# Kernel tuning notes

Hardware: AMD Instinct MI355X
Metric: run time of the kernel (lower is better)

Reference implementation:

```python
import jax, jax.numpy as jnp
import numpy as np

N, D, H, F, T = 2048, 256, 4, 64, 64
HF = H * F


def setup_inputs() -> dict:
    key = jax.random.key(0)
    ks = jax.random.split(key, 24)
    f32 = jnp.float32
    emb = jax.random.normal(ks[0], (N, D), f32)
    y_as_x = jax.random.normal(ks[1], (N, T), f32)
    adj = (jax.random.uniform(ks[2], (N, N)) < 0.02).astype(f32)
    u = lambda k, shape, s: jax.random.uniform(k, shape, f32, -s, s)
    stdv = 1.0 / np.sqrt(HF)
    inp = dict(emb=emb, y_as_x=y_as_x, adj=adj)
    for i, p in enumerate(['pos', 'neg']):
        o = 3 + i * 6
        inp[p + '_w'] = u(ks[o], (D, HF), stdv)
        inp[p + '_wu'] = u(ks[o + 1], (H, F), 1.0)
        inp[p + '_wv'] = u(ks[o + 2], (H, F), 1.0)
        inp[p + '_b'] = u(ks[o + 3], (1, HF), stdv)
        inp[p + '_pw'] = u(ks[o + 4], (D, HF), 0.02)
        inp[p + '_pb'] = jnp.zeros((HF,), f32)
    inp['self_w'] = u(ks[15], (D, D), 0.02)
    inp['self_b'] = jnp.zeros((D,), f32)
    inp['mlp_pos_w'] = u(ks[16], (HF, D), 0.02)
    inp['mlp_pos_b'] = jnp.zeros((D,), f32)
    inp['mlp_neg_w'] = u(ks[17], (HF, D), 0.02)
    inp['mlp_neg_b'] = jnp.zeros((D,), f32)
    inp['sem_w1'] = u(ks[18], (D, D), 0.02)
    inp['sem_b1'] = jnp.zeros((D,), f32)
    inp['sem_w2'] = u(ks[19], (D, 1), 0.02)
    return inp


def _gat(x, mask, w, wu, wv, b, pw, pb):
    # x: [N,D], mask: [N,N] bool; multi-head GAT with dense masked softmax
    s = (x @ w).reshape(N, H, F).transpose(1, 0, 2)          # [H,N,F]
    f1 = jnp.einsum('hnf,hf->hn', s, wu)                     # u-score per node
    f2 = jnp.einsum('hnf,hf->hn', s, wv)                     # v-score per node
    logits = f1[:, None, :] + f2[:, :, None]                 # [H,N,N], i<-j
    logits = jax.nn.leaky_relu(logits, 0.2)
    masked = jnp.where(mask[None], logits, -1e9)
    attn = jnp.where(mask[None], jax.nn.softmax(masked, axis=2), 0.0)
    out = jnp.einsum('hij,hjf->hif', attn, s)                # [H,N,F]
    out = out.transpose(1, 0, 2).reshape(N, HF) + b
    return out + x @ pw + pb


def reference(emb, y_as_x, adj, pos_w, pos_wu, pos_wv, pos_b, pos_pw, pos_pb,
              neg_w, neg_wu, neg_wv, neg_b, neg_pw, neg_pb,
              self_w, self_b, mlp_pos_w, mlp_pos_b, mlp_neg_w, mlp_neg_b,
              sem_w1, sem_b1, sem_w2):
    # batched pairwise correlation (replaces the per-node Python loop)
    yc = y_as_x - y_as_x.mean(axis=1, keepdims=True)         # centered
    dot = yc @ yc.T                                          # [N,N]
    std = jnp.sqrt((yc ** 2).sum(axis=1) / (T - 1))          # torch std: ddof=1
    corr = dot / (std[:, None] * std[None, :])
    edge = adj != 0
    pos_mask = edge & (corr >= 0.1)
    neg_mask = edge & (corr < 0.1)

    pos_sup = _gat(emb, pos_mask, pos_w, pos_wu, pos_wv, pos_b, pos_pw, pos_pb)
    neg_sup = _gat(emb, neg_mask, neg_w, neg_wu, neg_wv, neg_b, neg_pw, neg_pb)

    sup = emb @ self_w + self_b
    pos_sup = pos_sup @ mlp_pos_w + mlp_pos_b
    neg_sup = neg_sup @ mlp_neg_w + mlp_neg_b

    all_emb = jnp.stack((sup, pos_sup, neg_sup), axis=1)     # [N,3,D]
    # semantic attention over the 3 relation channels
    wlog = jnp.tanh(all_emb @ sem_w1 + sem_b1) @ sem_w2      # [N,3,1]
    beta = jax.nn.softmax(wlog, axis=1)
    x = (beta * all_emb).sum(axis=1)                         # [N,D]
    # PairNorm PN-SI
    x = x - x.mean(axis=0)
    rownorm = jnp.sqrt(1e-6 + (x ** 2).sum(axis=1, keepdims=True))
    return x / rownorm
```

## Files before the change

kernel.cpp:

```cpp
#include <hip/hip_runtime.h>
#include <hip/hip_bf16.h>

#define KN  2048
#define KD  256
#define KH  4
#define KF  64
#define KT  64

typedef __attribute__((ext_vector_type(8))) short short8;
typedef __attribute__((ext_vector_type(4))) float floatx4;

__device__ __forceinline__ float wave_sum(float v) {
    #pragma unroll
    for (int o = 32; o > 0; o >>= 1) v += __shfl_xor(v, o, 64);
    return v;
}
__device__ __forceinline__ float wave_max(float v) {
    #pragma unroll
    for (int o = 32; o > 0; o >>= 1) v = fmaxf(v, __shfl_xor(v, o, 64));
    return v;
}
__device__ __forceinline__ short f2bs(float x) {
    union { __hip_bfloat16 h; short s; } u;
    u.h = __float2bfloat16(x);
    return u.s;
}

__global__ __launch_bounds__(256) void setup_kernel(const float* __restrict__ y,
                                                    float* __restrict__ ycs,
                                                    float* __restrict__ colsum) {
    int blk = blockIdx.x;
    if (blk < 512) {
        int w = threadIdx.x >> 6, lane = threadIdx.x & 63;
        int n = blk * 4 + w;
        float v = y[n * KT + lane];
        float mean = wave_sum(v) * (1.0f / KT);
        float yc = v - mean;
        float ss = wave_sum(yc * yc);
        ycs[n * KT + lane] = yc * rsqrtf(ss * (1.0f / (KT - 1)));
    } else {
        for (int j = threadIdx.x; j < 8 * KD; j += 256) colsum[j] = 0.0f;
    }
}

__device__ __forceinline__ void corr_body(const float* __restrict__ ycs,
                                          const float* __restrict__ adj,
                                          unsigned char* __restrict__ code,
                                          int blk, char* smem) {
    float (*As)[68] = (float(*)[68])smem;
    float (*Bs)[68] = (float(*)[68])(smem + 4352);
    int t = threadIdx.x;
    int tx = t & 15, ty = t >> 4;
    int j0 = (blk & 31) * 64, i0 = (blk >> 5) * 64;
    int ar = t >> 2, ac = (t & 3) * 4;
    float acc[4][4] = {};
    for (int kt = 0; kt < KT; kt += 16) {
        float4 a4 = *reinterpret_cast<const float4*>(&ycs[(size_t)(i0 + ar) * KT + kt + ac]);
        float4 b4 = *reinterpret_cast<const float4*>(&ycs[(size_t)(j0 + ar) * KT + kt + ac]);
        As[ac + 0][ar] = a4.x; As[ac + 1][ar] = a4.y; As[ac + 2][ar] = a4.z; As[ac + 3][ar] = a4.w;
        Bs[ac + 0][ar] = b4.x; Bs[ac + 1][ar] = b4.y; Bs[ac + 2][ar] = b4.z; Bs[ac + 3][ar] = b4.w;
        __syncthreads();
        #pragma unroll
        for (int kk = 0; kk < 16; kk++) {
            float4 av = *reinterpret_cast<const float4*>(&As[kk][ty * 4]);
            float4 bv = *reinterpret_cast<const float4*>(&Bs[kk][tx * 4]);
            float a4v[4] = {av.x, av.y, av.z, av.w};
            float b4v[4] = {bv.x, bv.y, bv.z, bv.w};
            #pragma unroll
            for (int ii = 0; ii < 4; ii++)
                #pragma unroll
                for (int jj = 0; jj < 4; jj++) acc[ii][jj] += a4v[ii] * b4v[jj];
        }
        __syncthreads();
    }
    #pragma unroll
    for (int ii = 0; ii < 4; ii++) {
        int i = i0 + ty * 4 + ii;
        int jb = j0 + tx * 4;
        float4 av = *reinterpret_cast<const float4*>(&adj[(size_t)i * KN + jb]);
        float a4v[4] = {av.x, av.y, av.z, av.w};
        uchar4 cc;
        unsigned char* c = (unsigned char*)&cc;
        #pragma unroll
        for (int jj = 0; jj < 4; jj++)
            c[jj] = (a4v[jj] != 0.0f) ? ((acc[ii][jj] >= 0.1f) ? 1 : 2) : 0;
        *reinterpret_cast<uchar4*>(&code[(size_t)i * KN + jb]) = cc;
    }
}

template <bool TANH>
__device__ __forceinline__ void mfma_gemm_body(
    const float* __restrict__ A, int lda, int bm,
    const float* __restrict__ B, int ldb, int bn,
    const float* __restrict__ bias,
    float* __restrict__ C, int ldc, int cn, char* smem)
{
    short* As = (short*)smem;
    short* Bs = (short*)(smem + 5120);
    int t = threadIdx.x;
    int w = t >> 6, lane = t & 63;
    int m16 = lane & 15, kq = lane >> 4;
    floatx4 acc0 = {0,0,0,0}, acc1 = {0,0,0,0}, acc2 = {0,0,0,0}, acc3 = {0,0,0,0};
    int ar = t >> 2, acq = (t & 3) * 8;
    int bnn = t & 63, bkg = (t >> 6) * 8;
    for (int kt = 0; kt < KD; kt += 32) {
        const float* pa = &A[(size_t)(bm + ar) * lda + kt + acq];
        float4 a0 = *(const float4*)pa;
        float4 a1 = *(const float4*)(pa + 4);
        short8 av;
        av[0] = f2bs(a0.x); av[1] = f2bs(a0.y); av[2] = f2bs(a0.z); av[3] = f2bs(a0.w);
        av[4] = f2bs(a1.x); av[5] = f2bs(a1.y); av[6] = f2bs(a1.z); av[7] = f2bs(a1.w);
        const float* pb = &B[(size_t)(kt + bkg) * ldb + bn + bnn];
        short8 bv;
        #pragma unroll
        for (int u = 0; u < 8; u++) bv[u] = f2bs(pb[(size_t)u * ldb]);
        __syncthreads();
        *(short8*)&As[ar * 40 + acq] = av;
        *(short8*)&Bs[bnn * 40 + bkg] = bv;
        __syncthreads();
        short8 af  = *(short8*)&As[(w * 16 + m16) * 40 + kq * 8];
        short8 bf0 = *(short8*)&Bs[( 0 + m16) * 40 + kq * 8];
        short8 bf1 = *(short8*)&Bs[(16 + m16) * 40 + kq * 8];
        short8 bf2 = *(short8*)&Bs[(32 + m16) * 40 + kq * 8];
        short8 bf3 = *(short8*)&Bs[(48 + m16) * 40 + kq * 8];
        acc0 = __builtin_amdgcn_mfma_f32_16x16x32_bf16(af, bf0, acc0, 0, 0, 0);
        acc1 = __builtin_amdgcn_mfma_f32_16x16x32_bf16(af, bf1, acc1, 0, 0, 0);
        acc2 = __builtin_amdgcn_mfma_f32_16x16x32_bf16(af, bf2, acc2, 0, 0, 0);
        acc3 = __builtin_amdgcn_mfma_f32_16x16x32_bf16(af, bf3, acc3, 0, 0, 0);
    }
    int row0 = bm + w * 16 + kq * 4;
    floatx4 accs[4] = {acc0, acc1, acc2, acc3};
    #pragma unroll
    for (int nb = 0; nb < 4; nb++) {
        #pragma unroll
        for (int r = 0; r < 4; r++) {
            int col = nb * 16 + m16;
            float v = accs[nb][r] + (bias ? bias[col] : 0.0f);
            if (TANH) {
                float vc = fminf(fmaxf(v, -9.0f), 9.0f);
                float ex = __expf(2.0f * vc);
                v = (ex - 1.0f) / (ex + 1.0f);
            }
            C[(size_t)(row0 + r) * ldc + cn + col] = v;
        }
    }
}

struct EmbPtrs { float *S_pos, *S_neg, *P_pos, *P_neg, *sup; };
__global__ __launch_bounds__(256) void phase1_kernel(
    const float* __restrict__ ycs, const float* __restrict__ adj,
    unsigned char* __restrict__ code,
    const float* __restrict__ emb,
    const float* __restrict__ pos_w, const float* __restrict__ neg_w,
    const float* __restrict__ pos_pw, const float* __restrict__ neg_pw,
    const float* __restrict__ self_w,
    const float* __restrict__ pos_pb, const float* __restrict__ neg_pb,
    const float* __restrict__ self_b,
    EmbPtrs ep)
{
    __shared__ alignas(16) char smem[10240];
    int blk = blockIdx.x;
    if (blk < 1024) {
        corr_body(ycs, adj, code, blk, smem);
        return;
    }
    int b = blk - 1024;
    int tn = b % 20, tm = b / 20;
    int buf = tn >> 2, coloff = (tn & 3) * 64;
    const float* B; const float* bias; float* C;
    if (buf == 0)      { B = pos_w;  bias = nullptr;          C = ep.S_pos; }
    else if (buf == 1) { B = neg_w;  bias = nullptr;          C = ep.S_neg; }
    else if (buf == 2) { B = pos_pw; bias = pos_pb + coloff;  C = ep.P_pos; }
    else if (buf == 3) { B = neg_pw; bias = neg_pb + coloff;  C = ep.P_neg; }
    else               { B = self_w; bias = self_b + coloff;  C = ep.sup; }
    mfma_gemm_body<false>(emb, KD, tm * 64, B, KD, coloff, bias, C, KD, coloff, smem);
}

__global__ __launch_bounds__(256) void gemm_mlp(const float* __restrict__ Astack,
                                                const float* __restrict__ B0,
                                                const float* __restrict__ B1,
                                                const float* __restrict__ b0,
                                                const float* __restrict__ b1,
                                                float* __restrict__ Cstack) {
    __shared__ alignas(16) char smem[10240];
    int bm = blockIdx.y * 64;
    bool sel = bm >= KN;
    int cn = blockIdx.x * 64;
    mfma_gemm_body<false>(Astack, KD, bm, sel ? B1 : B0, KD, cn,
                          (sel ? b1 : b0) + cn, Cstack, KD, cn, smem);
}

__global__ __launch_bounds__(256) void gemm_sem(const float* __restrict__ Astack,
                                                const float* __restrict__ B,
                                                const float* __restrict__ bias,
                                                float* __restrict__ Cstack) {
    __shared__ alignas(16) char smem[10240];
    int cn = blockIdx.x * 64;
    mfma_gemm_body<true>(Astack, KD, blockIdx.y * 64, B, KD, cn,
                         bias + cn, Cstack, KD, cn, smem);
}

__global__ __launch_bounds__(256) void f1f2_kernel(const float* __restrict__ Sp,
                                                   const float* __restrict__ Sn,
                                                   const float* __restrict__ wup,
                                                   const float* __restrict__ wvp,
                                                   const float* __restrict__ wun,
                                                   const float* __restrict__ wvn,
                                                   float* __restrict__ f1p,
                                                   float* __restrict__ f2p,
                                                   float* __restrict__ f1n,
                                                   float* __restrict__ f2n) {
    int b = blockIdx.x;
    int rel = b >> 11;
    int n = b & (KN - 1);
    int h = threadIdx.x >> 6, lane = threadIdx.x & 63;
    const float* S = rel ? Sn : Sp;
    const float* wu = rel ? wun : wup;
    const float* wv = rel ? wvn : wvp;
    float* f1 = rel ? f1n : f1p;
    float* f2 = rel ? f2n : f2p;
    float v = S[(size_t)n * KD + h * KF + lane];
    float s1 = wave_sum(v * wu[h * KF + lane]);
    float s2 = wave_sum(v * wv[h * KF + lane]);
    if (lane == 0) { f1[h * KN + n] = s1; f2[h * KN + n] = s2; }
}

#define MAXE 256
__global__ __launch_bounds__(256) void attn_kernel(
    const unsigned char* __restrict__ code,
    const float* __restrict__ f1p, const float* __restrict__ f2p,
    const float* __restrict__ Sp, const float* __restrict__ Pp,
    const float* __restrict__ bp, float* __restrict__ Gp,
    const float* __restrict__ f1n, const float* __restrict__ f2n,
    const float* __restrict__ Sn, const float* __restrict__ Pn,
    const float* __restrict__ bn_, float* __restrict__ Gn)
{
    __shared__ alignas(16) int jl[MAXE];
    __shared__ alignas(16) float lg[KH][MAXE];
    __shared__ int cnt;
    int blk = blockIdx.x;
    int rel = blk >> 11;
    int i = blk & (KN - 1);
    unsigned char want = rel ? (unsigned char)2 : (unsigned char)1;
    const float* f1 = rel ? f1n : f1p;
    const float* f2 = rel ? f2n : f2p;
    const float* S  = rel ? Sn : Sp;
    const float* P  = rel ? Pn : Pp;
    const float* b  = rel ? bn_ : bp;
    float* G        = rel ? Gn : Gp;
    int w = threadIdx.x >> 6, lane = threadIdx.x & 63;
    if (threadIdx.x == 0) cnt = 0;
    __syncthreads();
    #pragma unroll
    for (int it = 0; it < 2; it++) {
        int base = w * 512 + it * 256;
        uchar4 cv = *reinterpret_cast<const uchar4*>(&code[(size_t)i * KN + base + lane * 4]);
        const unsigned char* ce = (const unsigned char*)&cv;
        #pragma unroll
        for (int e = 0; e < 4; e++) {
            bool p = (ce[e] == want);
            unsigned long long bal = __ballot(p);
            int tot = __popcll(bal);
            int basepos = 0;
            if (lane == 0 && tot) basepos = atomicAdd(&cnt, tot);
            basepos = __shfl(basepos, 0, 64);
            if (p) {
                int idx = basepos + __popcll(bal & ((1ull << lane) - 1ull));
                if (idx < MAXE) jl[idx] = base + lane * 4 + e;
            }
        }
    }
    __syncthreads();
    int count = cnt; if (count > MAXE) count = MAXE;
    int h = w;
    float f2i = f2[h * KN + i];
    float m = -1e30f;
    for (int k = lane; k < count; k += 64) {
        int j = jl[k];
        float x = f1[h * KN + j] + f2i;
        x = (x > 0.0f) ? x : 0.2f * x;
        lg[h][k] = x;
        m = fmaxf(m, x);
    }
    m = wave_max(m);
    float ps = 0.0f;
    for (int k = lane; k < count; k += 64) {
        float e = __expf(lg[h][k] - m);
        lg[h][k] = e;
        ps += e;
    }
    float denom = wave_sum(ps);
    const float* Sh = S + h * KF + lane;
    float acc = 0.0f;
    int k = 0;
    for (; k + 4 <= count; k += 4) {
        int4 j4 = *reinterpret_cast<const int4*>(&jl[k]);
        float4 w4 = *reinterpret_cast<const float4*>(&lg[h][k]);
        float s0 = Sh[(size_t)j4.x * KD];
        float s1 = Sh[(size_t)j4.y * KD];
        float s2 = Sh[(size_t)j4.z * KD];
        float s3 = Sh[(size_t)j4.w * KD];
        acc += w4.x * s0 + w4.y * s1 + w4.z * s2 + w4.w * s3;
    }
    for (; k < count; k++)
        acc += lg[h][k] * Sh[(size_t)jl[k] * KD];
    float outv = count ? acc * (1.0f / denom) : 0.0f;
    int col = h * KF + lane;
    G[(size_t)i * KD + col] = outv + b[col] + P[(size_t)i * KD + col];
}

__global__ __launch_bounds__(256) void combine_kernel(const float* __restrict__ T0,
                                                      const float* __restrict__ T1,
                                                      const float* __restrict__ T2,
                                                      const float* __restrict__ w2,
                                                      const float* __restrict__ sup,
                                                      const float* __restrict__ psup,
                                                      const float* __restrict__ nsup,
                                                      float* __restrict__ X,
                                                      float* __restrict__ colsum) {
    int n = blockIdx.x, d = threadIdx.x;
    size_t idx = (size_t)n * KD + d;
    float w2d = w2[d];
    float p0 = T0[idx] * w2d, p1 = T1[idx] * w2d, p2 = T2[idx] * w2d;
    __shared__ float sbuf[4][3];
    int wv = d >> 6, lane = d & 63;
    float s0 = wave_sum(p0), s1 = wave_sum(p1), s2 = wave_sum(p2);
    if (lane == 0) { sbuf[wv][0] = s0; sbuf[wv][1] = s1; sbuf[wv][2] = s2; }
    __syncthreads();
    float w0 = sbuf[0][0] + sbuf[1][0] + sbuf[2][0] + sbuf[3][0];
    float w1 = sbuf[0][1] + sbuf[1][1] + sbuf[2][1] + sbuf[3][1];
    float w2l = sbuf[0][2] + sbuf[1][2] + sbuf[2][2] + sbuf[3][2];
    float mm = fmaxf(w0, fmaxf(w1, w2l));
    float e0 = __expf(w0 - mm), e1 = __expf(w1 - mm), e2 = __expf(w2l - mm);
    float inv = 1.0f / (e0 + e1 + e2);
    float x = (e0 * inv) * sup[idx] + (e1 * inv) * psup[idx] + (e2 * inv) * nsup[idx];
    X[idx] = x;
    atomicAdd(&colsum[(n & 7) * KD + d], x);
}

__global__ __launch_bounds__(256) void final_kernel(const float* __restrict__ X,
                                                    const float* __restrict__ colsum,
                                                    float* __restrict__ out) {
    int n = blockIdx.x, d = threadIdx.x;
    float cs = 0.0f;
    #pragma unroll
    for (int r = 0; r < 8; r++) cs += colsum[r * KD + d];
    float mean = cs * (1.0f / KN);
    float xc = X[(size_t)n * KD + d] - mean;
    __shared__ float sbuf[4];
    int wv = d >> 6, lane = d & 63;
    float s = wave_sum(xc * xc);
    if (lane == 0) sbuf[wv] = s;
    __syncthreads();
    float ss = sbuf[0] + sbuf[1] + sbuf[2] + sbuf[3];
    out[(size_t)n * KD + d] = xc * rsqrtf(1e-6f + ss);
}

extern "C" void kernel_launch(void* const* d_in, const int* in_sizes, int n_in,
                              void* d_out, int out_size, void* d_ws, size_t ws_size,
                              hipStream_t stream) {
    typedef const float* fp;
    fp emb    = (fp)d_in[0];
    fp y_as_x = (fp)d_in[1];
    fp adj    = (fp)d_in[2];
    fp pos_w  = (fp)d_in[3],  pos_wu = (fp)d_in[4],  pos_wv = (fp)d_in[5];
    fp pos_b  = (fp)d_in[6],  pos_pw = (fp)d_in[7],  pos_pb = (fp)d_in[8];
    fp neg_w  = (fp)d_in[9],  neg_wu = (fp)d_in[10], neg_wv = (fp)d_in[11];
    fp neg_b  = (fp)d_in[12], neg_pw = (fp)d_in[13], neg_pb = (fp)d_in[14];
    fp self_w = (fp)d_in[15], self_b = (fp)d_in[16];
    fp mlp_pos_w = (fp)d_in[17], mlp_pos_b = (fp)d_in[18];
    fp mlp_neg_w = (fp)d_in[19], mlp_neg_b = (fp)d_in[20];
    fp sem_w1 = (fp)d_in[21], sem_b1 = (fp)d_in[22], sem_w2 = (fp)d_in[23];
    float* out = (float*)d_out;

    char* ws = (char*)d_ws;
    float* ycs        = (float*)(ws + 0x0000000);
    unsigned char* cd = (unsigned char*)(ws + 0x0080000);
    float* S_pos      = (float*)(ws + 0x0480000);
    float* S_neg      = (float*)(ws + 0x0680000);
    float* P_pos      = (float*)(ws + 0x0880000);
    float* P_neg      = (float*)(ws + 0x0A80000);
    float* G_pos      = (float*)(ws + 0x0C80000);
    float* G_neg      = (float*)(ws + 0x0E80000);
    float* sup        = (float*)(ws + 0x1080000);
    float* psup       = (float*)(ws + 0x1280000);
    float* nsup       = (float*)(ws + 0x1480000);
    float* colsum     = (float*)(ws + 0x1680000);
    float* f1p        = (float*)(ws + 0x1700000);
    float* f2p        = (float*)(ws + 0x1708000);
    float* f1n        = (float*)(ws + 0x1710000);
    float* f2n        = (float*)(ws + 0x1718000);
    float* T0 = P_pos, *T1 = P_neg, *T2 = G_pos, *X = G_neg;

    setup_kernel<<<513, 256, 0, stream>>>(y_as_x, ycs, colsum);

    EmbPtrs ep = {S_pos, S_neg, P_pos, P_neg, sup};
    phase1_kernel<<<1024 + 640, 256, 0, stream>>>(ycs, adj, cd, emb,
                                                  pos_w, neg_w, pos_pw, neg_pw, self_w,
                                                  pos_pb, neg_pb, self_b, ep);

    f1f2_kernel<<<2 * KN, 256, 0, stream>>>(S_pos, S_neg, pos_wu, pos_wv, neg_wu, neg_wv,
                                            f1p, f2p, f1n, f2n);

    attn_kernel<<<2 * KN, 256, 0, stream>>>(cd,
                                            f1p, f2p, S_pos, P_pos, pos_b, G_pos,
                                            f1n, f2n, S_neg, P_neg, neg_b, G_neg);

    gemm_mlp<<<dim3(4, 64), 256, 0, stream>>>(G_pos, mlp_pos_w, mlp_neg_w,
                                              mlp_pos_b, mlp_neg_b, psup);
    gemm_sem<<<dim3(4, 96), 256, 0, stream>>>(sup, sem_w1, sem_b1, T0);

    combine_kernel<<<KN, 256, 0, stream>>>(T0, T1, T2, sem_w2, sup, psup, nsup, X, colsum);
    final_kernel<<<KN, 256, 0, stream>>>(X, colsum, out);
}
```

Baseline: 177.0 us.

## Fuse setup and f1f2 into phase1, vectorize attention gather, merge sem GEMM

The per-row centering and normalization of y now happens inside the correlation tiles, so the separate setup kernel goes away, and colsum zeroing moves into one extra phase1 block. The f1/f2 per-head score reduction is computed in the epilogue of the S GEMMs using wave shuffles, which removes the f1f2 kernel and its re-read of S. The semantic GEMM on `sup` now runs in the same launch as the MLP GEMM, leaving a smaller second sem launch. The attention gather loads float4 per lane across four neighbor groups, with the neighbor list padded to a multiple of four. Colsum atomics are spread over 32 slots instead of 8. Together these cut launches and memory passes, at the cost of redundant per-tile normalization work and more shuffle reductions.

Result: slower. 218.9 us (+23.7%).

```diff
diff --git a/kernel.cpp b/kernel.cpp
--- a/kernel.cpp
+++ b/kernel.cpp
@@ -6,6 +6,7 @@
 #define KH  4
 #define KF  64
 #define KT  64
+#define NCS 32
 
 typedef __attribute__((ext_vector_type(8))) short short8;
 typedef __attribute__((ext_vector_type(4))) float floatx4;
@@ -26,24 +27,7 @@
     return u.s;
 }
 
-__global__ __launch_bounds__(256) void setup_kernel(const float* __restrict__ y,
-                                                    float* __restrict__ ycs,
-                                                    float* __restrict__ colsum) {
-    int blk = blockIdx.x;
-    if (blk < 512) {
-        int w = threadIdx.x >> 6, lane = threadIdx.x & 63;
-        int n = blk * 4 + w;
-        float v = y[n * KT + lane];
-        float mean = wave_sum(v) * (1.0f / KT);
-        float yc = v - mean;
-        float ss = wave_sum(yc * yc);
-        ycs[n * KT + lane] = yc * rsqrtf(ss * (1.0f / (KT - 1)));
-    } else {
-        for (int j = threadIdx.x; j < 8 * KD; j += 256) colsum[j] = 0.0f;
-    }
-}
-
-__device__ __forceinline__ void corr_body(const float* __restrict__ ycs,
+__device__ __forceinline__ void corr_body(const float* __restrict__ y,
                                           const float* __restrict__ adj,
                                           unsigned char* __restrict__ code,
                                           int blk, char* smem) {
@@ -52,20 +36,53 @@
     int t = threadIdx.x;
     int tx = t & 15, ty = t >> 4;
     int j0 = (blk & 31) * 64, i0 = (blk >> 5) * 64;
-    int ar = t >> 2, ac = (t & 3) * 4;
+    int r = t >> 2, q = t & 3;
+    float4 ai[4], bj[4];
+    #pragma unroll
+    for (int c = 0; c < 4; c++) {
+        ai[c] = *reinterpret_cast<const float4*>(&y[(size_t)(i0 + r) * KT + c * 16 + q * 4]);
+        bj[c] = *reinterpret_cast<const float4*>(&y[(size_t)(j0 + r) * KT + c * 16 + q * 4]);
+    }
+    float sa = 0.0f, sa2 = 0.0f, sb = 0.0f, sb2 = 0.0f;
+    #pragma unroll
+    for (int c = 0; c < 4; c++) {
+        float av[4] = {ai[c].x, ai[c].y, ai[c].z, ai[c].w};
+        float bv[4] = {bj[c].x, bj[c].y, bj[c].z, bj[c].w};
+        #pragma unroll
+        for (int u = 0; u < 4; u++) {
+            sa += av[u]; sa2 += av[u] * av[u];
+            sb += bv[u]; sb2 += bv[u] * bv[u];
+        }
+    }
+    #pragma unroll
+    for (int o = 1; o < 4; o <<= 1) {
+        sa += __shfl_xor(sa, o, 64);  sa2 += __shfl_xor(sa2, o, 64);
+        sb += __shfl_xor(sb, o, 64);  sb2 += __shfl_xor(sb2, o, 64);
+    }
+    float ma = sa * (1.0f / KT), mb = sb * (1.0f / KT);
+    float inva = rsqrtf((sa2 - KT * ma * ma) * (1.0f / (KT - 1)));
+    float invb = rsqrtf((sb2 - KT * mb * mb) * (1.0f / (KT - 1)));
+    #pragma unroll
+    for (int c = 0; c < 4; c++) {
+        ai[c].x = (ai[c].x - ma) * inva; ai[c].y = (ai[c].y - ma) * inva;
+        ai[c].z = (ai[c].z - ma) * inva; ai[c].w = (ai[c].w - ma) * inva;
+        bj[c].x = (bj[c].x - mb) * invb; bj[c].y = (bj[c].y - mb) * invb;
+        bj[c].z = (bj[c].z - mb) * invb; bj[c].w = (bj[c].w - mb) * invb;
+    }
     float acc[4][4] = {};
-    for (int kt = 0; kt < KT; kt += 16) {
-        float4 a4 = *reinterpret_cast<const float4*>(&ycs[(size_t)(i0 + ar) * KT + kt + ac]);
-        float4 b4 = *reinterpret_cast<const float4*>(&ycs[(size_t)(j0 + ar) * KT + kt + ac]);
-        As[ac + 0][ar] = a4.x; As[ac + 1][ar] = a4.y; As[ac + 2][ar] = a4.z; As[ac + 3][ar] = a4.w;
-        Bs[ac + 0][ar] = b4.x; Bs[ac + 1][ar] = b4.y; Bs[ac + 2][ar] = b4.z; Bs[ac + 3][ar] = b4.w;
+    #pragma unroll
+    for (int c = 0; c < 4; c++) {
+        As[q * 4 + 0][r] = ai[c].x; As[q * 4 + 1][r] = ai[c].y;
+        As[q * 4 + 2][r] = ai[c].z; As[q * 4 + 3][r] = ai[c].w;
+        Bs[q * 4 + 0][r] = bj[c].x; Bs[q * 4 + 1][r] = bj[c].y;
+        Bs[q * 4 + 2][r] = bj[c].z; Bs[q * 4 + 3][r] = bj[c].w;
         __syncthreads();
         #pragma unroll
         for (int kk = 0; kk < 16; kk++) {
-            float4 av = *reinterpret_cast<const float4*>(&As[kk][ty * 4]);
-            float4 bv = *reinterpret_cast<const float4*>(&Bs[kk][tx * 4]);
-            float a4v[4] = {av.x, av.y, av.z, av.w};
-            float b4v[4] = {bv.x, bv.y, bv.z, bv.w};
+            float4 av4 = *reinterpret_cast<const float4*>(&As[kk][ty * 4]);
+            float4 bv4 = *reinterpret_cast<const float4*>(&Bs[kk][tx * 4]);
+            float a4v[4] = {av4.x, av4.y, av4.z, av4.w};
+            float b4v[4] = {bv4.x, bv4.y, bv4.z, bv4.w};
             #pragma unroll
             for (int ii = 0; ii < 4; ii++)
                 #pragma unroll
@@ -77,8 +94,8 @@
     for (int ii = 0; ii < 4; ii++) {
         int i = i0 + ty * 4 + ii;
         int jb = j0 + tx * 4;
-        float4 av = *reinterpret_cast<const float4*>(&adj[(size_t)i * KN + jb]);
-        float a4v[4] = {av.x, av.y, av.z, av.w};
+        float4 av4 = *reinterpret_cast<const float4*>(&adj[(size_t)i * KN + jb]);
+        float a4v[4] = {av4.x, av4.y, av4.z, av4.w};
         uchar4 cc;
         unsigned char* c = (unsigned char*)&cc;
         #pragma unroll
@@ -93,7 +110,10 @@
     const float* __restrict__ A, int lda, int bm,
     const float* __restrict__ B, int ldb, int bn,
     const float* __restrict__ bias,
-    float* __restrict__ C, int ldc, int cn, char* smem)
+    float* __restrict__ C, int ldc, int cn,
+    float* __restrict__ f1h, float* __restrict__ f2h,
+    const float* __restrict__ wu_h, const float* __restrict__ wv_h,
+    char* smem)
 {
     short* As = (short*)smem;
     short* Bs = (short*)(smem + 5120);
@@ -144,11 +164,30 @@
             C[(size_t)(row0 + r) * ldc + cn + col] = v;
         }
     }
-}
-
-struct EmbPtrs { float *S_pos, *S_neg, *P_pos, *P_neg, *sup; };
+    if (f1h) {
+        float wuv[4], wvv[4];
+        #pragma unroll
+        for (int nb = 0; nb < 4; nb++) { wuv[nb] = wu_h[nb * 16 + m16]; wvv[nb] = wv_h[nb * 16 + m16]; }
+        #pragma unroll
+        for (int r = 0; r < 4; r++) {
+            float p1 = accs[0][r] * wuv[0] + accs[1][r] * wuv[1] + accs[2][r] * wuv[2] + accs[3][r] * wuv[3];
+            float p2 = accs[0][r] * wvv[0] + accs[1][r] * wvv[1] + accs[2][r] * wvv[2] + accs[3][r] * wvv[3];
+            #pragma unroll
+            for (int o = 1; o < 16; o <<= 1) {
+                p1 += __shfl_xor(p1, o, 64);
+                p2 += __shfl_xor(p2, o, 64);
+            }
+            if (m16 == 0) { f1h[row0 + r] = p1; f2h[row0 + r] = p2; }
+        }
+    }
+}
+
+struct EmbPtrs {
+    float *S_pos, *S_neg, *P_pos, *P_neg, *sup;
+    float *f1p, *f2p, *f1n, *f2n;
+};
 __global__ __launch_bounds__(256) void phase1_kernel(
-    const float* __restrict__ ycs, const float* __restrict__ adj,
+    const float* __restrict__ y, const float* __restrict__ adj,
     unsigned char* __restrict__ code,
     const float* __restrict__ emb,
     const float* __restrict__ pos_w, const float* __restrict__ neg_w,
@@ -156,24 +195,40 @@
     const float* __restrict__ self_w,
     const float* __restrict__ pos_pb, const float* __restrict__ neg_pb,
     const float* __restrict__ self_b,
-    EmbPtrs ep)
+    const float* __restrict__ pos_wu, const float* __restrict__ pos_wv,
+    const float* __restrict__ neg_wu, const float* __restrict__ neg_wv,
+    float* __restrict__ colsum, EmbPtrs ep)
 {
     __shared__ alignas(16) char smem[10240];
     int blk = blockIdx.x;
     if (blk < 1024) {
-        corr_body(ycs, adj, code, blk, smem);
+        corr_body(y, adj, code, blk, smem);
+        return;
+    }
+    if (blk >= 1664) {
+        for (int j = threadIdx.x; j < NCS * KD; j += 256) colsum[j] = 0.0f;
         return;
     }
     int b = blk - 1024;
     int tn = b % 20, tm = b / 20;
     int buf = tn >> 2, coloff = (tn & 3) * 64;
+    int h = tn & 3;
     const float* B; const float* bias; float* C;
-    if (buf == 0)      { B = pos_w;  bias = nullptr;          C = ep.S_pos; }
-    else if (buf == 1) { B = neg_w;  bias = nullptr;          C = ep.S_neg; }
-    else if (buf == 2) { B = pos_pw; bias = pos_pb + coloff;  C = ep.P_pos; }
-    else if (buf == 3) { B = neg_pw; bias = neg_pb + coloff;  C = ep.P_neg; }
-    else               { B = self_w; bias = self_b + coloff;  C = ep.sup; }
-    mfma_gemm_body<false>(emb, KD, tm * 64, B, KD, coloff, bias, C, KD, coloff, smem);
+    float *f1h = nullptr, *f2h = nullptr;
+    const float *wu_h = nullptr, *wv_h = nullptr;
+    if (buf == 0) {
+        B = pos_w;  bias = nullptr; C = ep.S_pos;
+        f1h = ep.f1p + h * KN; f2h = ep.f2p + h * KN;
+        wu_h = pos_wu + h * KF; wv_h = pos_wv + h * KF;
+    } else if (buf == 1) {
+        B = neg_w;  bias = nullptr; C = ep.S_neg;
+        f1h = ep.f1n + h * KN; f2h = ep.f2n + h * KN;
+        wu_h = neg_wu + h * KF; wv_h = neg_wv + h * KF;
+    } else if (buf == 2) { B = pos_pw; bias = pos_pb + coloff;  C = ep.P_pos; }
+    else if (buf == 3)   { B = neg_pw; bias = neg_pb + coloff;  C = ep.P_neg; }
+    else                 { B = self_w; bias = self_b + coloff;  C = ep.sup; }
+    mfma_gemm_body<false>(emb, KD, tm * 64, B, KD, coloff, bias,
+                          C, KD, coloff, f1h, f2h, wu_h, wv_h, smem);
 }
 
 __global__ __launch_bounds__(256) void gemm_mlp(const float* __restrict__ Astack,
@@ -181,13 +236,26 @@
                                                 const float* __restrict__ B1,
                                                 const float* __restrict__ b0,
                                                 const float* __restrict__ b1,
-                                                float* __restrict__ Cstack) {
+                                                float* __restrict__ Cstack,
+                                                const float* __restrict__ sup,
+                                                const float* __restrict__ semw1,
+                                                const float* __restrict__ semb1,
+                                                float* __restrict__ T0) {
     __shared__ alignas(16) char smem[10240];
-    int bm = blockIdx.y * 64;
-    bool sel = bm >= KN;
+    int by = blockIdx.y;
     int cn = blockIdx.x * 64;
-    mfma_gemm_body<false>(Astack, KD, bm, sel ? B1 : B0, KD, cn,
-                          (sel ? b1 : b0) + cn, Cstack, KD, cn, smem);
+    if (by < 64) {
+        int bm = by * 64;
+        bool sel = bm >= KN;
+        mfma_gemm_body<false>(Astack, KD, bm, sel ? B1 : B0, KD, cn,
+                              (sel ? b1 : b0) + cn, Cstack, KD, cn,
+                              nullptr, nullptr, nullptr, nullptr, smem);
+    } else {
+        int bm = (by - 64) * 64;
+        mfma_gemm_body<true>(sup, KD, bm, semw1, KD, cn,
+                             semb1 + cn, T0, KD, cn,
+                             nullptr, nullptr, nullptr, nullptr, smem);
+    }
 }
 
 __global__ __launch_bounds__(256) void gemm_sem(const float* __restrict__ Astack,
@@ -197,32 +265,8 @@
     __shared__ alignas(16) char smem[10240];
     int cn = blockIdx.x * 64;
     mfma_gemm_body<true>(Astack, KD, blockIdx.y * 64, B, KD, cn,
-                         bias + cn, Cstack, KD, cn, smem);
-}
-
-__global__ __launch_bounds__(256) void f1f2_kernel(const float* __restrict__ Sp,
-                                                   const float* __restrict__ Sn,
-                                                   const float* __restrict__ wup,
-                                                   const float* __restrict__ wvp,
-                                                   const float* __restrict__ wun,
-                                                   const float* __restrict__ wvn,
-                                                   float* __restrict__ f1p,
-                                                   float* __restrict__ f2p,
-                                                   float* __restrict__ f1n,
-                                                   float* __restrict__ f2n) {
-    int b = blockIdx.x;
-    int rel = b >> 11;
-    int n = b & (KN - 1);
-    int h = threadIdx.x >> 6, lane = threadIdx.x & 63;
-    const float* S = rel ? Sn : Sp;
-    const float* wu = rel ? wun : wup;
-    const float* wv = rel ? wvn : wvp;
-    float* f1 = rel ? f1n : f1p;
-    float* f2 = rel ? f2n : f2p;
-    float v = S[(size_t)n * KD + h * KF + lane];
-    float s1 = wave_sum(v * wu[h * KF + lane]);
-    float s2 = wave_sum(v * wv[h * KF + lane]);
-    if (lane == 0) { f1[h * KN + n] = s1; f2[h * KN + n] = s2; }
+                         bias + cn, Cstack, KD, cn,
+                         nullptr, nullptr, nullptr, nullptr, smem);
 }
 
 #define MAXE 256
@@ -272,6 +316,9 @@
     }
     __syncthreads();
     int count = cnt; if (count > MAXE) count = MAXE;
+    int countR = (count + 3) & ~3;
+    if (threadIdx.x < countR - count) jl[count + threadIdx.x] = 0;
+    __syncthreads();
     int h = w;
     float f2i = f2[h * KN + i];
     float m = -1e30f;
@@ -290,23 +337,33 @@
         ps += e;
     }
     float denom = wave_sum(ps);
-    const float* Sh = S + h * KF + lane;
-    float acc = 0.0f;
-    int k = 0;
-    for (; k + 4 <= count; k += 4) {
-        int4 j4 = *reinterpret_cast<const int4*>(&jl[k]);
-        float4 w4 = *reinterpret_cast<const float4*>(&lg[h][k]);
-        float s0 = Sh[(size_t)j4.x * KD];
-        float s1 = Sh[(size_t)j4.y * KD];
-        float s2 = Sh[(size_t)j4.z * KD];
-        float s3 = Sh[(size_t)j4.w * KD];
-        acc += w4.x * s0 + w4.y * s1 + w4.z * s2 + w4.w * s3;
-    }
-    for (; k < count; k++)
-        acc += lg[h][k] * Sh[(size_t)jl[k] * KD];
-    float outv = count ? acc * (1.0f / denom) : 0.0f;
-    int col = h * KF + lane;
-    G[(size_t)i * KD + col] = outv + b[col] + P[(size_t)i * KD + col];
+    for (int k2 = count + lane; k2 < countR; k2 += 64) lg[h][k2] = 0.0f;
+    int g = lane >> 4, q4 = (lane & 15) * 4;
+    const float* Sh4 = S + h * KF + q4;
+    float ax = 0.0f, ay = 0.0f, az = 0.0f, aw = 0.0f;
+    for (int k = 0; k < countR; k += 4) {
+        int j = jl[k + g];
+        float wgt = lg[h][k + g];
+        float4 sv = *reinterpret_cast<const float4*>(&Sh4[(size_t)j * KD]);
+        ax += wgt * sv.x; ay += wgt * sv.y; az += wgt * sv.z; aw += wgt * sv.w;
+    }
+    #pragma unroll
+    for (int o = 16; o < 64; o <<= 1) {
+        ax += __shfl_xor(ax, o, 64); ay += __shfl_xor(ay, o, 64);
+        az += __shfl_xor(az, o, 64); aw += __shfl_xor(aw, o, 64);
+    }
+    if (g == 0) {
+        float inv = count ? (1.0f / denom) : 0.0f;
+        int col = h * KF + q4;
+        size_t idx = (size_t)i * KD + col;
+        float4 pv = *reinterpret_cast<const float4*>(&P[idx]);
+        float4 o4;
+        o4.x = ax * inv + b[col + 0] + pv.x;
+        o4.y = ay * inv + b[col + 1] + pv.y;
+        o4.z = az * inv + b[col + 2] + pv.z;
+        o4.w = aw * inv + b[col + 3] + pv.w;
+        *reinterpret_cast<float4*>(&G[idx]) = o4;
+    }
 }
 
 __global__ __launch_bounds__(256) void combine_kernel(const float* __restrict__ T0,
@@ -335,7 +392,7 @@
     float inv = 1.0f / (e0 + e1 + e2);
     float x = (e0 * inv) * sup[idx] + (e1 * inv) * psup[idx] + (e2 * inv) * nsup[idx];
     X[idx] = x;
-    atomicAdd(&colsum[(n & 7) * KD + d], x);
+    atomicAdd(&colsum[(n & (NCS - 1)) * KD + d], x);
 }
 
 __global__ __launch_bounds__(256) void final_kernel(const float* __restrict__ X,
@@ -344,7 +401,7 @@
     int n = blockIdx.x, d = threadIdx.x;
     float cs = 0.0f;
     #pragma unroll
-    for (int r = 0; r < 8; r++) cs += colsum[r * KD + d];
+    for (int r = 0; r < NCS; r++) cs += colsum[r * KD + d];
     float mean = cs * (1.0f / KN);
     float xc = X[(size_t)n * KD + d] - mean;
     __shared__ float sbuf[4];
@@ -374,7 +431,6 @@
     float* out = (float*)d_out;
 
     char* ws = (char*)d_ws;
-    float* ycs        = (float*)(ws + 0x0000000);
     unsigned char* cd = (unsigned char*)(ws + 0x0080000);
     float* S_pos      = (float*)(ws + 0x0480000);
     float* S_neg      = (float*)(ws + 0x0680000);
@@ -392,23 +448,21 @@
     float* f2n        = (float*)(ws + 0x1718000);
     float* T0 = P_pos, *T1 = P_neg, *T2 = G_pos, *X = G_neg;
 
-    setup_kernel<<<513, 256, 0, stream>>>(y_as_x, ycs, colsum);
-
-    EmbPtrs ep = {S_pos, S_neg, P_pos, P_neg, sup};
-    phase1_kernel<<<1024 + 640, 256, 0, stream>>>(ycs, adj, cd, emb,
-                                                  pos_w, neg_w, pos_pw, neg_pw, self_w,
-                                                  pos_pb, neg_pb, self_b, ep);
-
-    f1f2_kernel<<<2 * KN, 256, 0, stream>>>(S_pos, S_neg, pos_wu, pos_wv, neg_wu, neg_wv,
-                                            f1p, f2p, f1n, f2n);
+    EmbPtrs ep = {S_pos, S_neg, P_pos, P_neg, sup, f1p, f2p, f1n, f2n};
+    phase1_kernel<<<1024 + 640 + 1, 256, 0, stream>>>(y_as_x, adj, cd, emb,
+                                                      pos_w, neg_w, pos_pw, neg_pw, self_w,
+                                                      pos_pb, neg_pb, self_b,
+                                                      pos_wu, pos_wv, neg_wu, neg_wv,
+                                                      colsum, ep);
 
     attn_kernel<<<2 * KN, 256, 0, stream>>>(cd,
                                             f1p, f2p, S_pos, P_pos, pos_b, G_pos,
                                             f1n, f2n, S_neg, P_neg, neg_b, G_neg);
 
-    gemm_mlp<<<dim3(4, 64), 256, 0, stream>>>(G_pos, mlp_pos_w, mlp_neg_w,
-                                              mlp_pos_b, mlp_neg_b, psup);
-    gemm_sem<<<dim3(4, 96), 256, 0, stream>>>(sup, sem_w1, sem_b1, T0);
+    gemm_mlp<<<dim3(4, 96), 256, 0, stream>>>(G_pos, mlp_pos_w, mlp_neg_w,
+                                              mlp_pos_b, mlp_neg_b, psup,
+                                              sup, sem_w1, sem_b1, T0);
+    gemm_sem<<<dim3(4, 64), 256, 0, stream>>>(psup, sem_w1, sem_b1, T1);
 
     combine_kernel<<<KN, 256, 0, stream>>>(T0, T1, T2, sem_w2, sup, psup, nsup, X, colsum);
     final_kernel<<<KN, 256, 0, stream>>>(X, colsum, out);
```
